# Performance work log

Hardware: AMD Instinct MI355X
Metric: run time of the kernel (lower is better)

Reference implementation:

```python
import jax, jax.numpy as jnp
import numpy as np

B, T, C = 2, 2048, 1024
NUM_HEADS = 16
HEAD_DIM = C // NUM_HEADS
TEMP = 1.0
LN_EPS = 1e-6


def setup_inputs() -> dict:
    key = jax.random.key(0)
    kx, kqw, kpw = jax.random.split(key, 3)
    x = jax.random.normal(kx, (B, T, C), dtype=jnp.float32)
    # causal mask, broadcastable to [B, H, T, T]
    mask = jnp.tril(jnp.ones((T, T), dtype=bool))[None, None, :, :]
    # LayerNorm params (flax defaults: scale=1, bias=0)
    ln_scale = jnp.ones((C,), dtype=jnp.float32)
    ln_bias = jnp.zeros((C,), dtype=jnp.float32)
    # xavier_uniform init for dense kernels, zero bias (torch_linear)
    lim_qkv = float(np.sqrt(6.0 / (C + 3 * C)))
    qkv_w = jax.random.uniform(kqw, (C, 3 * C), jnp.float32, -lim_qkv, lim_qkv)
    qkv_b = jnp.zeros((3 * C,), dtype=jnp.float32)
    lim_p = float(np.sqrt(6.0 / (C + C)))
    proj_w = jax.random.uniform(kpw, (C, C), jnp.float32, -lim_p, lim_p)
    proj_b = jnp.zeros((C,), dtype=jnp.float32)
    return {"x": x, "mask": mask, "ln_scale": ln_scale, "ln_bias": ln_bias,
            "qkv_w": qkv_w, "qkv_b": qkv_b, "proj_w": proj_w, "proj_b": proj_b}


def reference(x, mask, ln_scale, ln_bias, qkv_w, qkv_b, proj_w, proj_b):
    b, t, c = x.shape
    # LayerNorm (eps=1e-6, flax default)
    mu = jnp.mean(x, axis=-1, keepdims=True)
    var = jnp.mean(jnp.square(x - mu), axis=-1, keepdims=True)
    xn = (x - mu) * jax.lax.rsqrt(var + LN_EPS) * ln_scale + ln_bias
    # fused QKV projection
    qkv = xn @ qkv_w + qkv_b
    q, k, v = jnp.split(qkv, 3, axis=-1)
    q = q.reshape(b, t, NUM_HEADS, HEAD_DIM) / TEMP
    k = k.reshape(b, t, NUM_HEADS, HEAD_DIM)
    v = v.reshape(b, t, NUM_HEADS, HEAD_DIM)
    # scaled dot-product attention with mask (eval path: no dropout)
    q = q / jnp.sqrt(jnp.float32(HEAD_DIM)).astype(x.dtype)
    scores = jnp.einsum('bqhd,bkhd->bhqk', q, k)  # [B,H,T,T]
    big_neg = jnp.finfo(x.dtype).min
    scores = jnp.where(mask, scores, big_neg)
    attn_weights = jax.nn.softmax(scores, axis=-1).astype(x.dtype)
    out = jnp.einsum('bhqk,bkhd->bqhd', attn_weights, v).reshape(b, t, c)
    return out @ proj_w + proj_b
```

## Files before the change

### kernel.cpp

```cpp
#include <hip/hip_runtime.h>
#include <cstdint>

#define DEV __device__ __forceinline__

typedef unsigned int u32;
typedef unsigned short u16;
typedef __attribute__((ext_vector_type(4))) float f32x4;
typedef __attribute__((ext_vector_type(4))) u32 u32x4;
typedef __attribute__((ext_vector_type(2))) u32 u32x2;
typedef __attribute__((ext_vector_type(8))) __bf16 bf16x8;

static_assert(sizeof(bf16x8) == 16, "bf16x8 must be 16B");

static constexpr int Tn = 2048, Cn = 1024, Hn = 16;
static constexpr int Mrows = 2 * Tn;
static constexpr float QSCALE = 0.125f;

DEV u16 f2bf_rne(float f) {
  u32 u = __builtin_bit_cast(u32, f);
  u32 r = u + 0x7fffu + ((u >> 16) & 1u);
  return (u16)(r >> 16);
}
DEV float bf2f(u16 h) {
  u32 u = ((u32)h) << 16;
  return __builtin_bit_cast(float, u);
}

DEV void stage16(const void* g, void* l) {
#if __has_builtin(__builtin_amdgcn_global_load_lds)
  __builtin_amdgcn_global_load_lds(
      (__attribute__((address_space(1))) u32*)(uintptr_t)g,
      (__attribute__((address_space(3))) u32*)l, 16, 0, 0);
#else
  *(u32x4*)l = *(const u32x4*)g;
#endif
}

__global__ __launch_bounds__(256) void ln_kernel(const float* __restrict__ x,
                                                 const float* __restrict__ sc,
                                                 const float* __restrict__ bi,
                                                 u16* __restrict__ xn) {
  int row = blockIdx.x;
  int t = threadIdx.x;
  const float* xr = x + (size_t)row * Cn;
  f32x4 v = *(const f32x4*)(xr + t * 4);
  float s = v.x + v.y + v.z + v.w;
  float s2 = v.x * v.x + v.y * v.y + v.z * v.z + v.w * v.w;
#pragma unroll
  for (int off = 1; off < 64; off <<= 1) {
    s += __shfl_xor(s, off);
    s2 += __shfl_xor(s2, off);
  }
  __shared__ float red[8];
  if ((t & 63) == 0) {
    red[(t >> 6) * 2] = s;
    red[(t >> 6) * 2 + 1] = s2;
  }
  __syncthreads();
  s = red[0] + red[2] + red[4] + red[6];
  s2 = red[1] + red[3] + red[5] + red[7];
  float mean = s * (1.0f / Cn);
  float var = s2 * (1.0f / Cn) - mean * mean;
  float rstd = rsqrtf(var + 1e-6f);
  f32x4 g = *(const f32x4*)(sc + t * 4);
  f32x4 b = *(const f32x4*)(bi + t * 4);
  u32 lo = (u32)f2bf_rne((v.x - mean) * rstd * g.x + b.x) |
           ((u32)f2bf_rne((v.y - mean) * rstd * g.y + b.y) << 16);
  u32 hi = (u32)f2bf_rne((v.z - mean) * rstd * g.z + b.z) |
           ((u32)f2bf_rne((v.w - mean) * rstd * g.w + b.w) << 16);
  u32x2 pack = {lo, hi};
  *(u32x2*)(xn + (size_t)row * Cn + t * 4) = pack;
}

__global__ __launch_bounds__(256) void transpose_cast(const float* __restrict__ src,
                                                      u16* __restrict__ dst,
                                                      int R, int Cc) {
  __shared__ float tile[32][33];
  int tx = threadIdx.x, ty = threadIdx.y;
  int c0 = blockIdx.x * 32, r0 = blockIdx.y * 32;
#pragma unroll
  for (int k = 0; k < 4; ++k)
    tile[ty + 8 * k][tx] = src[(size_t)(r0 + ty + 8 * k) * Cc + c0 + tx];
  __syncthreads();
#pragma unroll
  for (int k = 0; k < 4; ++k)
    dst[(size_t)(c0 + ty + 8 * k) * R + r0 + tx] = f2bf_rne(tile[tx][ty + 8 * k]);
}

template <bool OUT_F32>
__global__ __launch_bounds__(256, 2) void gemm_kernel(const u16* __restrict__ A,
                                                      const u16* __restrict__ Bt,
                                                      const float* __restrict__ bias,
                                                      void* __restrict__ Cout,
                                                      int Nsz, int Ksz) {
  __shared__ u16 As[128 * 32];
  __shared__ u16 Bs[128 * 32];
  int t = threadIdx.x;
  int l = t & 63, w = t >> 6;
  int quad = l >> 4, c16 = l & 15;
  int wm = w & 1, wn = w >> 1;
  int m0 = blockIdx.y * 128, n0 = blockIdx.x * 128;

  f32x4 acc[4][4];
#pragma unroll
  for (int mt = 0; mt < 4; ++mt)
#pragma unroll
    for (int nt = 0; nt < 4; ++nt) acc[mt][nt] = (f32x4){0.f, 0.f, 0.f, 0.f};

  for (int kk = 0; kk < Ksz; kk += 32) {
#pragma unroll
    for (int i = 0; i < 2; ++i) {
      int c = t + i * 256;
      int m = c >> 2, k8 = (c & 3) ^ ((m >> 1) & 3);
      stage16(A + (size_t)(m0 + m) * Ksz + kk + k8 * 8, (char*)As + c * 16);
    }
#pragma unroll
    for (int i = 0; i < 2; ++i) {
      int c = t + i * 256;
      int n = c >> 2, k8 = (c & 3) ^ ((n >> 1) & 3);
      stage16(Bt + (size_t)(n0 + n) * Ksz + kk + k8 * 8, (char*)Bs + c * 16);
    }
    __syncthreads();
    bf16x8 af[4], bf[4];
#pragma unroll
    for (int mt = 0; mt < 4; ++mt) {
      int m = wm * 64 + mt * 16 + c16;
      int LC = m * 4 + (quad ^ ((m >> 1) & 3));
      af[mt] = *(const bf16x8*)((const char*)As + LC * 16);
    }
#pragma unroll
    for (int nt = 0; nt < 4; ++nt) {
      int n = wn * 64 + nt * 16 + c16;
      int LC = n * 4 + (quad ^ ((n >> 1) & 3));
      bf[nt] = *(const bf16x8*)((const char*)Bs + LC * 16);
    }
#pragma unroll
    for (int mt = 0; mt < 4; ++mt)
#pragma unroll
      for (int nt = 0; nt < 4; ++nt)
        acc[mt][nt] = __builtin_amdgcn_mfma_f32_16x16x32_bf16(af[mt], bf[nt],
                                                              acc[mt][nt], 0, 0, 0);
    __syncthreads();
  }
#pragma unroll
  for (int mt = 0; mt < 4; ++mt) {
    int row = m0 + wm * 64 + mt * 16 + quad * 4;
#pragma unroll
    for (int nt = 0; nt < 4; ++nt) {
      int col = n0 + wn * 64 + nt * 16 + c16;
      float bv = bias[col];
#pragma unroll
      for (int r = 0; r < 4; ++r) {
        float v = acc[mt][nt][r] + bv;
        if (OUT_F32)
          ((float*)Cout)[(size_t)(row + r) * Nsz + col] = v;
        else
          ((u16*)Cout)[(size_t)(row + r) * Nsz + col] = f2bf_rne(v);
      }
    }
  }
}

__global__ __launch_bounds__(256, 2) void flash_kernel(const u16* __restrict__ qkv,
                                                       u16* __restrict__ aout) {
  int qt = (int)gridDim.x - 1 - (int)blockIdx.x;
  int bh = blockIdx.y;
  int b = bh >> 4, h = bh & 15;
  int t = threadIdx.x, l = t & 63, w = t >> 6;
  int quad = l >> 4, c16 = l & 15;
  int q0 = qt * 128;

  __shared__ u16 Ks[128 * 64];
  __shared__ u32 Vt[64 * 66];

  bf16x8 qf[2][2];
#pragma unroll
  for (int nt = 0; nt < 2; ++nt)
#pragma unroll
    for (int ks = 0; ks < 2; ++ks) {
      int q = q0 + w * 32 + nt * 16 + c16;
      const u16* g = qkv + (size_t)(b * Tn + q) * 3072 + h * 64 + ks * 32 + quad * 8;
      u32x4 raw = *(const u32x4*)g;
      u32x4 out;
#pragma unroll
      for (int i = 0; i < 4; ++i) {
        float lo = bf2f((u16)(raw[i] & 0xffff)) * QSCALE;
        float hi = bf2f((u16)(raw[i] >> 16)) * QSCALE;
        out[i] = (u32)f2bf_rne(lo) | ((u32)f2bf_rne(hi) << 16);
      }
      qf[nt][ks] = __builtin_bit_cast(bf16x8, out);
    }

  float mrow[2] = {-1e30f, -1e30f};
  float lrow[2] = {0.f, 0.f};
  f32x4 o[2][4];
#pragma unroll
  for (int mq = 0; mq < 2; ++mq)
#pragma unroll
    for (int dt = 0; dt < 4; ++dt) o[mq][dt] = (f32x4){0.f, 0.f, 0.f, 0.f};

  for (int kt = 0; kt <= qt; ++kt) {
#pragma unroll
    for (int i = 0; i < 4; ++i) {
      int c = t + i * 256;
      int key = c >> 3, d8 = (c & 7) ^ (key & 7);
      stage16(qkv + (size_t)(b * Tn + kt * 128 + key) * 3072 + Cn + h * 64 + d8 * 8,
              (char*)Ks + c * 16);
    }
#pragma unroll
    for (int i = 0; i < 4; ++i) {
      int c = t + i * 256;
      int key = c >> 3, d8 = c & 7;
      u32x4 v = *(const u32x4*)(qkv + (size_t)(b * Tn + kt * 128 + key) * 3072 +
                                2 * Cn + h * 64 + d8 * 8);
      u32x4 p;
#pragma unroll
      for (int j = 0; j < 4; ++j) p[j] = (u32)__shfl_xor((int)v[j], 8);
      int odd = key & 1;
      int jbase = odd ? 4 : 0;
#pragma unroll
      for (int jj = 0; jj < 4; ++jj) {
        int j = jbase + jj;
        u32 mj = v[j >> 1], pj = p[j >> 1];
        u16 mine = (j & 1) ? (u16)(mj >> 16) : (u16)(mj & 0xffff);
        u16 thrs = (j & 1) ? (u16)(pj >> 16) : (u16)(pj & 0xffff);
        u32 word = odd ? ((u32)thrs | ((u32)mine << 16))
                       : ((u32)mine | ((u32)thrs << 16));
        Vt[(d8 * 8 + j) * 66 + ((key >> 1) & 63)] = word;
      }
    }
    __syncthreads();

    f32x4 s[8][2];
#pragma unroll
    for (int mt = 0; mt < 8; ++mt)
#pragma unroll
      for (int nt = 0; nt < 2; ++nt) s[mt][nt] = (f32x4){0.f, 0.f, 0.f, 0.f};
#pragma unroll
    for (int mt = 0; mt < 8; ++mt) {
#pragma unroll
      for (int ks = 0; ks < 2; ++ks) {
        int key = mt * 16 + c16;
        int d8 = ks * 4 + quad;
        int LC = key * 8 + (d8 ^ (key & 7));
        bf16x8 kf = *(const bf16x8*)((const char*)Ks + LC * 16);
#pragma unroll
        for (int nt = 0; nt < 2; ++nt)
          s[mt][nt] = __builtin_amdgcn_mfma_f32_16x16x32_bf16(kf, qf[nt][ks],
                                                              s[mt][nt], 0, 0, 0);
      }
    }
    if (kt == qt) {
#pragma unroll
      for (int mt = 0; mt < 8; ++mt)
#pragma unroll
        for (int nt = 0; nt < 2; ++nt)
#pragma unroll
          for (int r = 0; r < 4; ++r) {
            int key = kt * 128 + mt * 16 + quad * 4 + r;
            int q = q0 + w * 32 + nt * 16 + c16;
            if (key > q) s[mt][nt][r] = -1e30f;
          }
    }
    float alph[2];
#pragma unroll
    for (int nt = 0; nt < 2; ++nt) {
      float rm = -1e30f;
#pragma unroll
      for (int mt = 0; mt < 8; ++mt)
#pragma unroll
        for (int r = 0; r < 4; ++r) rm = fmaxf(rm, s[mt][nt][r]);
      rm = fmaxf(rm, __shfl_xor(rm, 16));
      rm = fmaxf(rm, __shfl_xor(rm, 32));
      float mnew = fmaxf(mrow[nt], rm);
      alph[nt] = __expf(mrow[nt] - mnew);
      mrow[nt] = mnew;
      float rs = 0.f;
#pragma unroll
      for (int mt = 0; mt < 8; ++mt)
#pragma unroll
        for (int r = 0; r < 4; ++r) {
          float e = __expf(s[mt][nt][r] - mnew);
          s[mt][nt][r] = e;
          rs += e;
        }
      rs += __shfl_xor(rs, 16);
      rs += __shfl_xor(rs, 32);
      lrow[nt] = lrow[nt] * alph[nt] + rs;
    }
#pragma unroll
    for (int mq = 0; mq < 2; ++mq)
#pragma unroll
      for (int r = 0; r < 4; ++r) {
        float a = __shfl(alph[mq], quad * 4 + r);
#pragma unroll
        for (int dt = 0; dt < 4; ++dt) o[mq][dt][r] *= a;
      }
#pragma unroll
    for (int ks = 0; ks < 4; ++ks) {
#pragma unroll
      for (int mq = 0; mq < 2; ++mq) {
        u32 packed[4];
#pragma unroll
        for (int r = 0; r < 4; ++r)
          packed[r] = (u32)f2bf_rne(s[ks * 2][mq][r]) |
                      ((u32)f2bf_rne(s[ks * 2 + 1][mq][r]) << 16);
        u32 words[4];
#pragma unroll
        for (int j = 0; j < 8; ++j) {
          int srcq = ((quad & 1) << 1) + (j >> 2);
          u32 pj = (u32)__shfl((int)packed[j & 3], (srcq << 4) + c16);
          u16 valj = (quad & 2) ? (u16)(pj >> 16) : (u16)(pj & 0xffff);
          if ((j & 1) == 0)
            words[j >> 1] = valj;
          else
            words[j >> 1] |= ((u32)valj) << 16;
        }
        u32x4 wv = {words[0], words[1], words[2], words[3]};
        bf16x8 pa = __builtin_bit_cast(bf16x8, wv);
#pragma unroll
        for (int dt = 0; dt < 4; ++dt) {
          int d = dt * 16 + c16;
          const u32* vp = &Vt[d * 66 + ks * 16 + quad * 4];
          u32x2 w0 = *(const u32x2*)vp;
          u32x2 w1 = *(const u32x2*)(vp + 2);
          u32x4 vv = {w0.x, w0.y, w1.x, w1.y};
          bf16x8 vf = __builtin_bit_cast(bf16x8, vv);
          o[mq][dt] = __builtin_amdgcn_mfma_f32_16x16x32_bf16(pa, vf, o[mq][dt],
                                                              0, 0, 0);
        }
      }
    }
    __syncthreads();
  }

  float linv[2] = {1.0f / lrow[0], 1.0f / lrow[1]};
#pragma unroll
  for (int mq = 0; mq < 2; ++mq)
#pragma unroll
    for (int r = 0; r < 4; ++r) {
      float li = __shfl(linv[mq], quad * 4 + r);
      int q = q0 + w * 32 + mq * 16 + quad * 4 + r;
      size_t rowg = (size_t)(b * Tn + q);
#pragma unroll
      for (int dt = 0; dt < 4; ++dt) {
        int col = h * 64 + dt * 16 + c16;
        aout[rowg * 1024 + col] = f2bf_rne(o[mq][dt][r] * li);
      }
    }
}

extern "C" void kernel_launch(void* const* d_in, const int* in_sizes, int n_in,
                              void* d_out, int out_size, void* d_ws, size_t ws_size,
                              hipStream_t stream) {
  const float* x = (const float*)d_in[0];
  const float* ln_s = (const float*)d_in[2];
  const float* ln_b = (const float*)d_in[3];
  const float* qkv_w = (const float*)d_in[4];
  const float* qkv_b = (const float*)d_in[5];
  const float* proj_w = (const float*)d_in[6];
  const float* proj_b = (const float*)d_in[7];
  float* out = (float*)d_out;
  char* ws = (char*)d_ws;

  u16* xn = (u16*)ws;
  u16* wqkv = (u16*)(ws + (8ull << 20));
  u16* wproj = (u16*)(ws + (14ull << 20));
  u16* qkvm = (u16*)(ws + (16ull << 20));
  u16* attn = (u16*)(ws + (40ull << 20));

  ln_kernel<<<Mrows, 256, 0, stream>>>(x, ln_s, ln_b, xn);
  transpose_cast<<<dim3(96, 32), dim3(32, 8), 0, stream>>>(qkv_w, wqkv, 1024, 3072);
  transpose_cast<<<dim3(32, 32), dim3(32, 8), 0, stream>>>(proj_w, wproj, 1024, 1024);
  gemm_kernel<false><<<dim3(24, 32), 256, 0, stream>>>(xn, wqkv, qkv_b, qkvm, 3072, 1024);
  flash_kernel<<<dim3(16, 32), 256, 0, stream>>>(qkvm, attn);
  gemm_kernel<true><<<dim3(8, 32), 256, 0, stream>>>(attn, wproj, proj_b, out, 1024, 1024);
}
```

Measured before the change: 265.3 us.

## Split long causal query tiles across blocks and pre-transpose V for flash attention

```diff
diff --git a/kernel.cpp b/kernel.cpp
--- a/kernel.cpp
+++ b/kernel.cpp
@@ -12,9 +12,8 @@
 
 static_assert(sizeof(bf16x8) == 16, "bf16x8 must be 16B");
 
-static constexpr int Tn = 2048, Cn = 1024, Hn = 16;
+static constexpr int Tn = 2048, Cn = 1024;
 static constexpr int Mrows = 2 * Tn;
-static constexpr float QSCALE = 0.125f;
 
 DEV u16 f2bf_rne(float f) {
   u32 u = __builtin_bit_cast(u32, f);
@@ -24,6 +23,9 @@
 DEV float bf2f(u16 h) {
   u32 u = ((u32)h) << 16;
   return __builtin_bit_cast(float, u);
+}
+DEV u32 pack2bf(float a, float b) {
+  return (u32)f2bf_rne(a) | ((u32)f2bf_rne(b) << 16);
 }
 
 DEV void stage16(const void* g, void* l) {
@@ -64,10 +66,8 @@
   float rstd = rsqrtf(var + 1e-6f);
   f32x4 g = *(const f32x4*)(sc + t * 4);
   f32x4 b = *(const f32x4*)(bi + t * 4);
-  u32 lo = (u32)f2bf_rne((v.x - mean) * rstd * g.x + b.x) |
-           ((u32)f2bf_rne((v.y - mean) * rstd * g.y + b.y) << 16);
-  u32 hi = (u32)f2bf_rne((v.z - mean) * rstd * g.z + b.z) |
-           ((u32)f2bf_rne((v.w - mean) * rstd * g.w + b.w) << 16);
+  u32 lo = pack2bf((v.x - mean) * rstd * g.x + b.x, (v.y - mean) * rstd * g.y + b.y);
+  u32 hi = pack2bf((v.z - mean) * rstd * g.z + b.z, (v.w - mean) * rstd * g.w + b.w);
   u32x2 pack = {lo, hi};
   *(u32x2*)(xn + (size_t)row * Cn + t * 4) = pack;
 }
@@ -87,7 +87,24 @@
     dst[(size_t)(c0 + ty + 8 * k) * R + r0 + tx] = f2bf_rne(tile[tx][ty + 8 * k]);
 }
 
-template <bool OUT_F32>
+__global__ __launch_bounds__(256) void vt_prep(const u16* __restrict__ qkvm,
+                                               u16* __restrict__ vt) {
+  __shared__ u16 tile[32][33];
+  int bh = blockIdx.z;
+  int b = bh >> 4, h = bh & 15;
+  int t0 = blockIdx.x * 32, d0 = blockIdx.y * 32;
+  int tx = threadIdx.x, ty = threadIdx.y;
+#pragma unroll
+  for (int k = 0; k < 4; ++k)
+    tile[ty + 8 * k][tx] =
+        qkvm[(size_t)(b * Tn + t0 + ty + 8 * k) * 3072 + 2 * Cn + h * 64 + d0 + tx];
+  __syncthreads();
+#pragma unroll
+  for (int k = 0; k < 4; ++k)
+    vt[((size_t)bh * 64 + d0 + ty + 8 * k) * 2048 + t0 + tx] = tile[tx][ty + 8 * k];
+}
+
+template <bool OUT_F32, bool QKV_SCALE>
 __global__ __launch_bounds__(256, 2) void gemm_kernel(const u16* __restrict__ A,
                                                       const u16* __restrict__ Bt,
                                                       const float* __restrict__ bias,
@@ -149,9 +166,10 @@
     for (int nt = 0; nt < 4; ++nt) {
       int col = n0 + wn * 64 + nt * 16 + c16;
       float bv = bias[col];
+      float scale = (QKV_SCALE && col < 1024) ? 0.125f : 1.0f;
 #pragma unroll
       for (int r = 0; r < 4; ++r) {
-        float v = acc[mt][nt][r] + bv;
+        float v = (acc[mt][nt][r] + bv) * scale;
         if (OUT_F32)
           ((float*)Cout)[(size_t)(row + r) * Nsz + col] = v;
         else
@@ -161,35 +179,41 @@
   }
 }
 
+__constant__ int4 chunk_tab[24] = {
+    {15, 0, 8, 0}, {15, 8, 8, 1}, {14, 0, 8, 0}, {7, 0, 8, -1},
+    {14, 8, 7, 1}, {13, 0, 7, 0}, {13, 7, 7, 1}, {12, 0, 7, 0}, {6, 0, 7, -1},
+    {12, 7, 6, 1}, {11, 0, 6, 0}, {11, 6, 6, 1}, {10, 0, 6, 0}, {5, 0, 6, -1},
+    {10, 6, 5, 1}, {9, 0, 5, 0}, {9, 5, 5, 1}, {8, 0, 5, 0}, {4, 0, 5, -1},
+    {8, 5, 4, 1}, {3, 0, 4, -1},
+    {2, 0, 3, -1},
+    {1, 0, 2, -1},
+    {0, 0, 1, -1}};
+
 __global__ __launch_bounds__(256, 2) void flash_kernel(const u16* __restrict__ qkv,
-                                                       u16* __restrict__ aout) {
-  int qt = (int)gridDim.x - 1 - (int)blockIdx.x;
-  int bh = blockIdx.y;
+                                                       const u16* __restrict__ vt,
+                                                       u16* __restrict__ aout,
+                                                       u16* __restrict__ Op,
+                                                       float* __restrict__ ml) {
+  int4 ck = chunk_tab[blockIdx.x >> 5];
+  int bh = blockIdx.x & 31;
+  int qt = ck.x, k0 = ck.y, kend = ck.y + ck.z, half = ck.w;
   int b = bh >> 4, h = bh & 15;
   int t = threadIdx.x, l = t & 63, w = t >> 6;
   int quad = l >> 4, c16 = l & 15;
   int q0 = qt * 128;
 
   __shared__ u16 Ks[128 * 64];
-  __shared__ u32 Vt[64 * 66];
+  __shared__ u16 Vs[64 * 128];
+  __shared__ u16 Ps[128 * 128];
 
   bf16x8 qf[2][2];
 #pragma unroll
   for (int nt = 0; nt < 2; ++nt)
 #pragma unroll
-    for (int ks = 0; ks < 2; ++ks) {
-      int q = q0 + w * 32 + nt * 16 + c16;
-      const u16* g = qkv + (size_t)(b * Tn + q) * 3072 + h * 64 + ks * 32 + quad * 8;
-      u32x4 raw = *(const u32x4*)g;
-      u32x4 out;
-#pragma unroll
-      for (int i = 0; i < 4; ++i) {
-        float lo = bf2f((u16)(raw[i] & 0xffff)) * QSCALE;
-        float hi = bf2f((u16)(raw[i] >> 16)) * QSCALE;
-        out[i] = (u32)f2bf_rne(lo) | ((u32)f2bf_rne(hi) << 16);
-      }
-      qf[nt][ks] = __builtin_bit_cast(bf16x8, out);
-    }
+    for (int ks = 0; ks < 2; ++ks)
+      qf[nt][ks] = *(const bf16x8*)(qkv +
+          (size_t)(b * Tn + q0 + w * 32 + nt * 16 + c16) * 3072 +
+          h * 64 + ks * 32 + quad * 8);
 
   float mrow[2] = {-1e30f, -1e30f};
   float lrow[2] = {0.f, 0.f};
@@ -199,7 +223,7 @@
 #pragma unroll
     for (int dt = 0; dt < 4; ++dt) o[mq][dt] = (f32x4){0.f, 0.f, 0.f, 0.f};
 
-  for (int kt = 0; kt <= qt; ++kt) {
+  for (int kt = k0; kt < kend; ++kt) {
 #pragma unroll
     for (int i = 0; i < 4; ++i) {
       int c = t + i * 256;
@@ -210,24 +234,9 @@
 #pragma unroll
     for (int i = 0; i < 4; ++i) {
       int c = t + i * 256;
-      int key = c >> 3, d8 = c & 7;
-      u32x4 v = *(const u32x4*)(qkv + (size_t)(b * Tn + kt * 128 + key) * 3072 +
-                                2 * Cn + h * 64 + d8 * 8);
-      u32x4 p;
-#pragma unroll
-      for (int j = 0; j < 4; ++j) p[j] = (u32)__shfl_xor((int)v[j], 8);
-      int odd = key & 1;
-      int jbase = odd ? 4 : 0;
-#pragma unroll
-      for (int jj = 0; jj < 4; ++jj) {
-        int j = jbase + jj;
-        u32 mj = v[j >> 1], pj = p[j >> 1];
-        u16 mine = (j & 1) ? (u16)(mj >> 16) : (u16)(mj & 0xffff);
-        u16 thrs = (j & 1) ? (u16)(pj >> 16) : (u16)(pj & 0xffff);
-        u32 word = odd ? ((u32)thrs | ((u32)mine << 16))
-                       : ((u32)mine | ((u32)thrs << 16));
-        Vt[(d8 * 8 + j) * 66 + ((key >> 1) & 63)] = word;
-      }
+      int d = c >> 4, k8 = (c & 15) ^ (d & 15);
+      stage16(vt + ((size_t)bh * 64 + d) * 2048 + kt * 128 + k8 * 8,
+              (char*)Vs + c * 16);
     }
     __syncthreads();
 
@@ -297,57 +306,99 @@
         for (int dt = 0; dt < 4; ++dt) o[mq][dt][r] *= a;
       }
 #pragma unroll
+    for (int mt = 0; mt < 8; ++mt)
+#pragma unroll
+      for (int nt = 0; nt < 2; ++nt) {
+        int q = w * 32 + nt * 16 + c16;
+        int kc = mt * 4 + quad;
+        int LC = q * 32 + (kc ^ ((q & 15) << 1));
+        u32x2 pk = {pack2bf(s[mt][nt][0], s[mt][nt][1]),
+                    pack2bf(s[mt][nt][2], s[mt][nt][3])};
+        *(u32x2*)((char*)Ps + LC * 8) = pk;
+      }
+#pragma unroll
     for (int ks = 0; ks < 4; ++ks) {
+      bf16x8 pa[2];
 #pragma unroll
       for (int mq = 0; mq < 2; ++mq) {
-        u32 packed[4];
-#pragma unroll
-        for (int r = 0; r < 4; ++r)
-          packed[r] = (u32)f2bf_rne(s[ks * 2][mq][r]) |
-                      ((u32)f2bf_rne(s[ks * 2 + 1][mq][r]) << 16);
-        u32 words[4];
-#pragma unroll
-        for (int j = 0; j < 8; ++j) {
-          int srcq = ((quad & 1) << 1) + (j >> 2);
-          u32 pj = (u32)__shfl((int)packed[j & 3], (srcq << 4) + c16);
-          u16 valj = (quad & 2) ? (u16)(pj >> 16) : (u16)(pj & 0xffff);
-          if ((j & 1) == 0)
-            words[j >> 1] = valj;
-          else
-            words[j >> 1] |= ((u32)valj) << 16;
-        }
-        u32x4 wv = {words[0], words[1], words[2], words[3]};
-        bf16x8 pa = __builtin_bit_cast(bf16x8, wv);
-#pragma unroll
-        for (int dt = 0; dt < 4; ++dt) {
-          int d = dt * 16 + c16;
-          const u32* vp = &Vt[d * 66 + ks * 16 + quad * 4];
-          u32x2 w0 = *(const u32x2*)vp;
-          u32x2 w1 = *(const u32x2*)(vp + 2);
-          u32x4 vv = {w0.x, w0.y, w1.x, w1.y};
-          bf16x8 vf = __builtin_bit_cast(bf16x8, vv);
-          o[mq][dt] = __builtin_amdgcn_mfma_f32_16x16x32_bf16(pa, vf, o[mq][dt],
+        int q = w * 32 + mq * 16 + c16;
+        int kc = ks * 8 + quad * 2;
+        int LC = q * 32 + (kc ^ ((q & 15) << 1));
+        pa[mq] = *(const bf16x8*)((const char*)Ps + LC * 8);
+      }
+#pragma unroll
+      for (int dt = 0; dt < 4; ++dt) {
+        int d = dt * 16 + c16;
+        int vc = d * 16 + ((ks * 4 + quad) ^ (d & 15));
+        bf16x8 vf = *(const bf16x8*)((const char*)Vs + vc * 16);
+#pragma unroll
+        for (int mq = 0; mq < 2; ++mq)
+          o[mq][dt] = __builtin_amdgcn_mfma_f32_16x16x32_bf16(pa[mq], vf, o[mq][dt],
                                                               0, 0, 0);
-        }
       }
     }
     __syncthreads();
   }
 
   float linv[2] = {1.0f / lrow[0], 1.0f / lrow[1]};
-#pragma unroll
-  for (int mq = 0; mq < 2; ++mq)
-#pragma unroll
-    for (int r = 0; r < 4; ++r) {
-      float li = __shfl(linv[mq], quad * 4 + r);
-      int q = q0 + w * 32 + mq * 16 + quad * 4 + r;
-      size_t rowg = (size_t)(b * Tn + q);
-#pragma unroll
-      for (int dt = 0; dt < 4; ++dt) {
-        int col = h * 64 + dt * 16 + c16;
-        aout[rowg * 1024 + col] = f2bf_rne(o[mq][dt][r] * li);
-      }
-    }
+  if (half < 0) {
+#pragma unroll
+    for (int mq = 0; mq < 2; ++mq)
+#pragma unroll
+      for (int r = 0; r < 4; ++r) {
+        float li = __shfl(linv[mq], quad * 4 + r);
+        int q = q0 + w * 32 + mq * 16 + quad * 4 + r;
+#pragma unroll
+        for (int dt = 0; dt < 4; ++dt)
+          aout[(size_t)(b * Tn + q) * 1024 + h * 64 + dt * 16 + c16] =
+              f2bf_rne(o[mq][dt][r] * li);
+      }
+  } else {
+    int ps = ((qt - 8) * 32 + bh) * 2 + half;
+#pragma unroll
+    for (int mq = 0; mq < 2; ++mq)
+#pragma unroll
+      for (int r = 0; r < 4; ++r) {
+        float li = __shfl(linv[mq], quad * 4 + r);
+        int qr = w * 32 + mq * 16 + quad * 4 + r;
+#pragma unroll
+        for (int dt = 0; dt < 4; ++dt)
+          Op[((size_t)ps * 128 + qr) * 64 + dt * 16 + c16] =
+              f2bf_rne(o[mq][dt][r] * li);
+      }
+    if (quad == 0) {
+#pragma unroll
+      for (int nt = 0; nt < 2; ++nt) {
+        int qr = w * 32 + nt * 16 + c16;
+        ml[((size_t)ps * 128 + qr) * 2] = mrow[nt];
+        ml[((size_t)ps * 128 + qr) * 2 + 1] = lrow[nt];
+      }
+    }
+  }
+}
+
+__global__ __launch_bounds__(256) void combine_kernel(const u16* __restrict__ Op,
+                                                      const float* __restrict__ ml,
+                                                      u16* __restrict__ aout) {
+  int qt = 8 + (blockIdx.x >> 5);
+  int bh = blockIdx.x & 31;
+  int b = bh >> 4, h = bh & 15;
+  int ps0 = ((qt - 8) * 32 + bh) * 2;
+  int d = threadIdx.x & 63, rq = threadIdx.x >> 6;
+  for (int r = 0; r < 32; ++r) {
+    int row = rq * 32 + r;
+    float m0 = ml[((size_t)ps0 * 128 + row) * 2];
+    float l0 = ml[((size_t)ps0 * 128 + row) * 2 + 1];
+    float m1 = ml[((size_t)(ps0 + 1) * 128 + row) * 2];
+    float l1 = ml[((size_t)(ps0 + 1) * 128 + row) * 2 + 1];
+    float M = fmaxf(m0, m1);
+    float w0 = __expf(m0 - M) * l0, w1 = __expf(m1 - M) * l1;
+    float inv = 1.0f / (w0 + w1);
+    float o0 = bf2f(Op[((size_t)ps0 * 128 + row) * 64 + d]);
+    float o1 = bf2f(Op[((size_t)(ps0 + 1) * 128 + row) * 64 + d]);
+    aout[(size_t)(b * Tn + qt * 128 + row) * 1024 + h * 64 + d] =
+        f2bf_rne((w0 * o0 + w1 * o1) * inv);
+  }
 }
 
 extern "C" void kernel_launch(void* const* d_in, const int* in_sizes, int n_in,
@@ -368,11 +419,18 @@
   u16* wproj = (u16*)(ws + (14ull << 20));
   u16* qkvm = (u16*)(ws + (16ull << 20));
   u16* attn = (u16*)(ws + (40ull << 20));
+  u16* vt = (u16*)(ws + (48ull << 20));
+  u16* Op = (u16*)ws;
+  float* ml = (float*)(ws + (8ull << 20));
 
   ln_kernel<<<Mrows, 256, 0, stream>>>(x, ln_s, ln_b, xn);
   transpose_cast<<<dim3(96, 32), dim3(32, 8), 0, stream>>>(qkv_w, wqkv, 1024, 3072);
   transpose_cast<<<dim3(32, 32), dim3(32, 8), 0, stream>>>(proj_w, wproj, 1024, 1024);
-  gemm_kernel<false><<<dim3(24, 32), 256, 0, stream>>>(xn, wqkv, qkv_b, qkvm, 3072, 1024);
-  flash_kernel<<<dim3(16, 32), 256, 0, stream>>>(qkvm, attn);
-  gemm_kernel<true><<<dim3(8, 32), 256, 0, stream>>>(attn, wproj, proj_b, out, 1024, 1024);
-}
+  gemm_kernel<false, true><<<dim3(24, 32), 256, 0, stream>>>(xn, wqkv, qkv_b, qkvm,
+                                                             3072, 1024);
+  vt_prep<<<dim3(64, 2, 32), dim3(32, 8), 0, stream>>>(qkvm, vt);
+  flash_kernel<<<768, 256, 0, stream>>>(qkvm, vt, attn, Op, ml);
+  combine_kernel<<<256, 256, 0, stream>>>(Op, ml, attn);
+  gemm_kernel<true, false><<<dim3(8, 32), 256, 0, stream>>>(attn, wproj, proj_b, out,
+                                                            1024, 1024);
+}
```

After: 224.1 us. -15.6%, faster.
